# Performance work log

Hardware: AMD Instinct MI355X
Metric: run time of the kernel (lower is better)

The kernel has to match this reference:

```python
import jax, jax.numpy as jnp
import numpy as np

TEMP = 0.05
NUM_CLUSTERS = 8192  # labels.max()+1 in the original; fixed for jit-compat
EPS_SUM = 1e-6

def _l2norm(x):
    # F.normalize(x, dim=1): x / ||x||.clamp_min(1e-12)
    return x / jnp.maximum(jnp.linalg.norm(x, axis=1, keepdims=True), 1e-12)

def setup_inputs() -> dict:
    key = jax.random.key(0)
    k1, k2, k3, k4 = jax.random.split(key, 4)
    B, N, D = 1024, 131072, 256
    inputs = jax.random.normal(k1, (B, D), dtype=jnp.float32)
    features = jax.random.normal(k2, (N, D), dtype=jnp.float32)  # memory bank buffer
    indexes = jax.random.randint(k3, (B,), 0, N)
    labels = jax.random.randint(k4, (N,), 0, NUM_CLUSTERS)
    return {"inputs": inputs, "features": features, "indexes": indexes, "labels": labels}

def reference(inputs, features, indexes, labels):
    B = inputs.shape[0]
    inputs_norm = _l2norm(inputs)            # [B, D]
    features_norm = _l2norm(features)        # [N, D]
    # HM.forward: cosine similarity against the memory bank, then temperature
    logits = (inputs_norm @ features_norm.T) / TEMP          # [B, N]
    # label-grouped scatter-reduce: sim[c, b] = sum over samples s with label c of logits[b, s]
    sim = jax.ops.segment_sum(logits.T, labels, num_segments=NUM_CLUSTERS)  # [NC, B]
    nums = jax.ops.segment_sum(jnp.ones((labels.shape[0],), jnp.float32), labels,
                               num_segments=NUM_CLUSTERS)                   # [NC]
    mask = (nums > 0).astype(jnp.float32)                                   # [NC]
    denom = mask * nums + (1.0 - mask)
    sim = sim / denom[:, None]               # per-cluster mean similarity
    # masked softmax over clusters, per sample
    simT = sim.T                             # [B, NC]
    exps = jnp.exp(simT) * mask[None, :]
    p = exps / (jnp.sum(exps, axis=1, keepdims=True) + EPS_SUM)
    logp = jnp.log(p + 1e-6)                 # [B, NC]
    targets = labels[indexes]                # [B]
    loss = -jnp.mean(jnp.take_along_axis(logp, targets[:, None], axis=1))
    return loss
```

## Files before the change

kernel.cpp:

```cpp
#include <hip/hip_runtime.h>

#define BSZ   1024
#define NSZ   131072
#define DSZ   256
#define NC    8192
#define TEMPR 0.05f
#define CAP   64

typedef float f32x4_t __attribute__((ext_vector_type(4)));
typedef int   i32x4_t __attribute__((ext_vector_type(4)));

__device__ __forceinline__ unsigned short f2bf(float f) {
  unsigned u = __float_as_uint(f);
  u += 0x7fffu + ((u >> 16) & 1u);
  return (unsigned short)(u >> 16);
}

__device__ __forceinline__ void gload16(const unsigned short* g, unsigned short* l) {
  __builtin_amdgcn_global_load_lds(
      (const __attribute__((address_space(1))) unsigned int*)(g),
      (__attribute__((address_space(3))) unsigned int*)(l), 16, 0, 0);
}

#define ZERO_F4_COUNT 2308

__global__ __launch_bounds__(256) void k_norm(const float* __restrict__ in,
                                              unsigned short* __restrict__ anorm,
                                              float4* __restrict__ zero_region) {
  int gid  = blockIdx.x * 256 + threadIdx.x;
  if (gid < ZERO_F4_COUNT) zero_region[gid] = make_float4(0.f, 0.f, 0.f, 0.f);
  int wid  = gid >> 6;
  int lane = threadIdx.x & 63;
  float4 v = reinterpret_cast<const float4*>(in)[wid * 64 + lane];
  float ss = v.x * v.x + v.y * v.y + v.z * v.z + v.w * v.w;
#pragma unroll
  for (int off = 32; off; off >>= 1) ss += __shfl_xor(ss, off);
  float rn = 1.f / fmaxf(sqrtf(ss), 1e-12f);
  ushort4 ob = make_ushort4(f2bf(v.x * rn), f2bf(v.y * rn), f2bf(v.z * rn), f2bf(v.w * rn));
  reinterpret_cast<ushort4*>(anorm)[wid * 64 + lane] = ob;
}

__global__ __launch_bounds__(256) void k_fill(const int* __restrict__ labels,
                                              int* __restrict__ cnt,
                                              int* __restrict__ bucket) {
  int i = blockIdx.x * 256 + threadIdx.x;
  int lab = labels[i];
  int p = atomicAdd(&cnt[lab], 1);
  if (p < CAP) bucket[(lab << 6) + p] = i;
}

__global__ __launch_bounds__(256) void k_gather_sum(const float* __restrict__ feat,
                                                    const int* __restrict__ bucket,
                                                    const int* __restrict__ cnt,
                                                    unsigned short* __restrict__ cmean) {
  __shared__ float4 part[192];
  int c    = blockIdx.x;
  int lane = threadIdx.x & 63;
  int wv   = threadIdx.x >> 6;
  int n = cnt[c];
  n = n < CAP ? n : CAP;
  int j = wv + 4 * lane;
  int myidx = (j < n) ? bucket[(c << 6) + j] : 0;
  float4 acc = make_float4(0.f, 0.f, 0.f, 0.f);
  int iters = (n - wv + 3) >> 2;
  float4 v;
  if (iters > 0) {
    int s0 = __shfl(myidx, 0);
    v = reinterpret_cast<const float4*>(feat)[(size_t)s0 * 64 + lane];
  }
  for (int t = 0; t < iters; ++t) {
    float4 cur = v;
    if (t + 1 < iters) {
      int sn = __shfl(myidx, t + 1);
      v = reinterpret_cast<const float4*>(feat)[(size_t)sn * 64 + lane];
    }
    float ss = cur.x * cur.x + cur.y * cur.y + cur.z * cur.z + cur.w * cur.w;
#pragma unroll
    for (int off = 32; off; off >>= 1) ss += __shfl_xor(ss, off);
    float rn = 1.f / fmaxf(sqrtf(ss), 1e-12f);
    acc.x += cur.x * rn; acc.y += cur.y * rn; acc.z += cur.z * rn; acc.w += cur.w * rn;
  }
  if (wv > 0) part[(wv - 1) * 64 + lane] = acc;
  __syncthreads();
  if (wv == 0) {
    float4 p1 = part[lane], p2 = part[64 + lane], p3 = part[128 + lane];
    acc.x += p1.x + p2.x + p3.x;
    acc.y += p1.y + p2.y + p3.y;
    acc.z += p1.z + p2.z + p3.z;
    acc.w += p1.w + p2.w + p3.w;
    float den = n > 0 ? (float)n : 1.f;
    float sc = 1.f / (TEMPR * den);
    ushort4 ob = make_ushort4(f2bf(acc.x * sc), f2bf(acc.y * sc),
                              f2bf(acc.z * sc), f2bf(acc.w * sc));
    reinterpret_cast<ushort4*>(cmean)[c * 64 + lane] = ob;
  }
}

__global__ __launch_bounds__(256) void k_gemm(const unsigned short* __restrict__ A,
                                              const unsigned short* __restrict__ Bt,
                                              const int* __restrict__ cnt,
                                              const int* __restrict__ indexes,
                                              const int* __restrict__ labels,
                                              float* __restrict__ sumexp,
                                              float* __restrict__ tlogit,
                                              int* __restrict__ ticket,
                                              float* __restrict__ out) {
  __shared__ __align__(16) unsigned short a_lds[128 * 64];
  __shared__ __align__(16) unsigned short b_lds[128 * 64];
  __shared__ int t_lds[128];
  __shared__ float red[4];
  __shared__ int lastflag;

  const int tid  = threadIdx.x;
  const int bn0  = blockIdx.x * 128;
  const int bm0  = blockIdx.y * 128;
  const int lane = tid & 63;
  const int w    = tid >> 6;
  const int wr   = w >> 1, wc = w & 1;
  const int col16 = lane & 15, khalf = lane >> 4;

  if (tid < 128) t_lds[tid] = labels[indexes[bm0 + tid]];

  f32x4_t acc[4][4] = {};

#pragma unroll 1
  for (int kt = 0; kt < 4; ++kt) {
    const int k0 = kt * 64;
    __syncthreads();
#pragma unroll
    for (int j = 0; j < 4; ++j) {
      int c   = (j * 4 + w) * 64 + lane;
      int row = c >> 3;
      int lk  = (c & 7) ^ (row & 7);
      const unsigned short* gA = A  + (size_t)(bm0 + row) * DSZ + k0 + lk * 8;
      const unsigned short* gB = Bt + (size_t)(bn0 + row) * DSZ + k0 + lk * 8;
      gload16(gA, a_lds + (j * 4 + w) * 512);
      gload16(gB, b_lds + (j * 4 + w) * 512);
    }
    __syncthreads();

#pragma unroll
    for (int ks = 0; ks < 2; ++ks) {
      const int klocB = ks * 64 + khalf * 16;
      i32x4_t af[4], bf[4];
#pragma unroll
      for (int m = 0; m < 4; ++m) {
        int lr = wr * 64 + m * 16 + col16;
        int ab = (lr << 7) + (klocB ^ ((lr & 7) << 4));
        af[m] = *reinterpret_cast<const i32x4_t*>(reinterpret_cast<const char*>(a_lds) + ab);
      }
#pragma unroll
      for (int n = 0; n < 4; ++n) {
        int lc = wc * 64 + n * 16 + col16;
        int bb = (lc << 7) + (klocB ^ ((lc & 7) << 4));
        bf[n] = *reinterpret_cast<const i32x4_t*>(reinterpret_cast<const char*>(b_lds) + bb);
      }
#pragma unroll
      for (int m = 0; m < 4; ++m)
#pragma unroll
        for (int n = 0; n < 4; ++n)
          asm("v_mfma_f32_16x16x32_bf16 %0, %1, %2, %0" : "+v"(acc[m][n]) : "v"(af[m]), "v"(bf[n]));
    }
  }

#pragma unroll
  for (int m = 0; m < 4; ++m) {
    const int lr0 = wr * 64 + m * 16 + khalf * 4;
    float s0 = 0.f, s1 = 0.f, s2 = 0.f, s3 = 0.f;
#pragma unroll
    for (int n = 0; n < 4; ++n) {
      int gc = bn0 + wc * 64 + n * 16 + col16;
      float msk = cnt[gc] > 0 ? 1.f : 0.f;
      if (t_lds[lr0 + 0] == gc) tlogit[bm0 + lr0 + 0] = acc[m][n][0];
      if (t_lds[lr0 + 1] == gc) tlogit[bm0 + lr0 + 1] = acc[m][n][1];
      if (t_lds[lr0 + 2] == gc) tlogit[bm0 + lr0 + 2] = acc[m][n][2];
      if (t_lds[lr0 + 3] == gc) tlogit[bm0 + lr0 + 3] = acc[m][n][3];
      s0 += msk * __expf(acc[m][n][0]);
      s1 += msk * __expf(acc[m][n][1]);
      s2 += msk * __expf(acc[m][n][2]);
      s3 += msk * __expf(acc[m][n][3]);
    }
#pragma unroll
    for (int off = 1; off < 16; off <<= 1) {
      s0 += __shfl_xor(s0, off);
      s1 += __shfl_xor(s1, off);
      s2 += __shfl_xor(s2, off);
      s3 += __shfl_xor(s3, off);
    }
    if (col16 == 0) {
      atomicAdd(&sumexp[bm0 + lr0 + 0], s0);
      atomicAdd(&sumexp[bm0 + lr0 + 1], s1);
      atomicAdd(&sumexp[bm0 + lr0 + 2], s2);
      atomicAdd(&sumexp[bm0 + lr0 + 3], s3);
    }
  }

  __syncthreads();
  if (tid == 0) {
    int t = __hip_atomic_fetch_add(ticket, 1, __ATOMIC_ACQ_REL, __HIP_MEMORY_SCOPE_AGENT);
    lastflag = (t == 511);
  }
  __syncthreads();
  if (lastflag) {
    float lp = 0.f;
    for (int r = tid; r < BSZ; r += 256) {
      float tl = __uint_as_float(__hip_atomic_load((const unsigned*)&tlogit[r],
                                 __ATOMIC_RELAXED, __HIP_MEMORY_SCOPE_AGENT));
      float se = __uint_as_float(__hip_atomic_load((const unsigned*)&sumexp[r],
                                 __ATOMIC_RELAXED, __HIP_MEMORY_SCOPE_AGENT));
      float p = __expf(tl) / (se + 1e-6f);
      lp += logf(p + 1e-6f);
    }
#pragma unroll
    for (int off = 32; off; off >>= 1) lp += __shfl_xor(lp, off);
    if (lane == 0) red[w] = lp;
    __syncthreads();
    if (tid == 0) out[0] = -(red[0] + red[1] + red[2] + red[3]) * (1.0f / (float)BSZ);
  }
}

#define OFF_ANORM   0u
#define OFF_CMEAN   524288u
#define OFF_BUCKET  (OFF_CMEAN + 4194304u)
#define OFF_TLOGIT  (OFF_BUCKET + 2097152u)
#define OFF_CNT     (OFF_TLOGIT + 4096u)
#define OFF_SUMEXP  (OFF_CNT + 32768u)
#define OFF_TICKET  (OFF_SUMEXP + 4096u)

extern "C" void kernel_launch(void* const* d_in, const int* in_sizes, int n_in,
                              void* d_out, int out_size, void* d_ws, size_t ws_size,
                              hipStream_t stream) {
  const float* inputs   = (const float*)d_in[0];
  const float* features = (const float*)d_in[1];
  const int*   indexes  = (const int*)d_in[2];
  const int*   labels   = (const int*)d_in[3];
  float* out = (float*)d_out;

  char* ws = (char*)d_ws;
  unsigned short* anorm   = (unsigned short*)(ws + OFF_ANORM);
  unsigned short* cmean   = (unsigned short*)(ws + OFF_CMEAN);
  int*            bucket  = (int*)(ws + OFF_BUCKET);
  float*          tlogit  = (float*)(ws + OFF_TLOGIT);
  int*            cnt     = (int*)(ws + OFF_CNT);
  float*          sumexp  = (float*)(ws + OFF_SUMEXP);
  int*            ticket  = (int*)(ws + OFF_TICKET);

  k_norm<<<256, 256, 0, stream>>>(inputs, anorm, (float4*)(ws + OFF_CNT));
  k_fill<<<NSZ / 256, 256, 0, stream>>>(labels, cnt, bucket);
  k_gather_sum<<<NC, 256, 0, stream>>>(features, bucket, cnt, cmean);
  k_gemm<<<dim3(NC / 128, BSZ / 128), 256, 0, stream>>>(anorm, cmean, cnt, indexes,
                                                        labels, sumexp, tlogit,
                                                        ticket, out);
}
```

Baseline: 68.26 us.

## Load GEMM fragments directly from global memory instead of staging through LDS

The GEMM kernel drops the LDS tiles, the global_load_lds staging and the block barriers. Each wave now loads its A and B MFMA fragments straight from global memory into registers, with the K loop fully unrolled over 8 steps. This removes barrier stalls and LDS traffic and lets the compiler issue many loads ahead of use. In exchange, each fragment is fetched redundantly by several waves through L1/L2 rather than shared in LDS, and register pressure goes up.

```diff
diff --git a/kernel.cpp b/kernel.cpp
--- a/kernel.cpp
+++ b/kernel.cpp
@@ -14,12 +14,6 @@
   unsigned u = __float_as_uint(f);
   u += 0x7fffu + ((u >> 16) & 1u);
   return (unsigned short)(u >> 16);
-}
-
-__device__ __forceinline__ void gload16(const unsigned short* g, unsigned short* l) {
-  __builtin_amdgcn_global_load_lds(
-      (const __attribute__((address_space(1))) unsigned int*)(g),
-      (__attribute__((address_space(3))) unsigned int*)(l), 16, 0, 0);
 }
 
 #define ZERO_F4_COUNT 2308
@@ -105,8 +99,6 @@
                                               float* __restrict__ tlogit,
                                               int* __restrict__ ticket,
                                               float* __restrict__ out) {
-  __shared__ __align__(16) unsigned short a_lds[128 * 64];
-  __shared__ __align__(16) unsigned short b_lds[128 * 64];
   __shared__ int t_lds[128];
   __shared__ float red[4];
   __shared__ int lastflag;
@@ -121,46 +113,26 @@
 
   if (tid < 128) t_lds[tid] = labels[indexes[bm0 + tid]];
 
+  const unsigned short* Abase = A  + (size_t)(bm0 + wr * 64 + col16) * DSZ + khalf * 8;
+  const unsigned short* Bbase = Bt + (size_t)(bn0 + wc * 64 + col16) * DSZ + khalf * 8;
+
   f32x4_t acc[4][4] = {};
 
-#pragma unroll 1
-  for (int kt = 0; kt < 4; ++kt) {
-    const int k0 = kt * 64;
-    __syncthreads();
-#pragma unroll
-    for (int j = 0; j < 4; ++j) {
-      int c   = (j * 4 + w) * 64 + lane;
-      int row = c >> 3;
-      int lk  = (c & 7) ^ (row & 7);
-      const unsigned short* gA = A  + (size_t)(bm0 + row) * DSZ + k0 + lk * 8;
-      const unsigned short* gB = Bt + (size_t)(bn0 + row) * DSZ + k0 + lk * 8;
-      gload16(gA, a_lds + (j * 4 + w) * 512);
-      gload16(gB, b_lds + (j * 4 + w) * 512);
-    }
-    __syncthreads();
-
-#pragma unroll
-    for (int ks = 0; ks < 2; ++ks) {
-      const int klocB = ks * 64 + khalf * 16;
-      i32x4_t af[4], bf[4];
-#pragma unroll
-      for (int m = 0; m < 4; ++m) {
-        int lr = wr * 64 + m * 16 + col16;
-        int ab = (lr << 7) + (klocB ^ ((lr & 7) << 4));
-        af[m] = *reinterpret_cast<const i32x4_t*>(reinterpret_cast<const char*>(a_lds) + ab);
-      }
-#pragma unroll
-      for (int n = 0; n < 4; ++n) {
-        int lc = wc * 64 + n * 16 + col16;
-        int bb = (lc << 7) + (klocB ^ ((lc & 7) << 4));
-        bf[n] = *reinterpret_cast<const i32x4_t*>(reinterpret_cast<const char*>(b_lds) + bb);
-      }
-#pragma unroll
-      for (int m = 0; m < 4; ++m)
-#pragma unroll
-        for (int n = 0; n < 4; ++n)
-          asm("v_mfma_f32_16x16x32_bf16 %0, %1, %2, %0" : "+v"(acc[m][n]) : "v"(af[m]), "v"(bf[n]));
-    }
+#pragma unroll
+  for (int s = 0; s < 8; ++s) {
+    const int ko = s * 32;
+    i32x4_t af[4], bf[4];
+#pragma unroll
+    for (int m = 0; m < 4; ++m)
+      af[m] = *reinterpret_cast<const i32x4_t*>(Abase + (size_t)m * 16 * DSZ + ko);
+#pragma unroll
+    for (int n = 0; n < 4; ++n)
+      bf[n] = *reinterpret_cast<const i32x4_t*>(Bbase + (size_t)n * 16 * DSZ + ko);
+#pragma unroll
+    for (int m = 0; m < 4; ++m)
+#pragma unroll
+      for (int n = 0; n < 4; ++n)
+        asm("v_mfma_f32_16x16x32_bf16 %0, %1, %2, %0" : "+v"(acc[m][n]) : "v"(af[m]), "v"(bf[n]));
   }
 
 #pragma unroll
```

Result: slower. 78.54 us (+15.1%).
